# Performance work log

Measured on AMD Instinct MI355X. Metric: run time of the kernel, lower is better.

Reference implementation:

```python
import jax, jax.numpy as jnp
import numpy as np

MAX_DIS = 15
PCD_RANGE = np.array([0.0, 0.0, 0.0, 30.0, 30.0, 14.0])
VOXEL = np.array([2.0, 2.0, 2.0])


def _make_locs():
    low, high = PCD_RANGE[:3], PCD_RANGE[3:]
    grid = ((high - low) // VOXEL + 1).astype(int)  # [16,16,8]
    axes = [low[i] + np.arange(grid[i]) * VOXEL[i] for i in range(3)]
    locs = np.stack(np.meshgrid(*axes, indexing='ij'), axis=-1).reshape(-1, 3)
    return jnp.asarray(locs, jnp.float32)  # [L=2048, 3]


def setup_inputs() -> dict:
    key = jax.random.key(0)
    low, high = PCD_RANGE[:3], PCD_RANGE[3:]
    pcd = jax.random.uniform(key, (4, 8192, 3), dtype=jnp.float32)
    pcd = pcd * jnp.asarray(high - low, jnp.float32) + jnp.asarray(low, jnp.float32)
    return {"pcd": pcd, "locs": _make_locs()}


def reference(pcd, locs):
    # pcd: [B, N, 3]; locs: [L, 3]
    # dis[l, b, n] = ceil(||pcd[b,n] - locs[l]||)
    diff = pcd[None, :, :, :] - locs[:, None, None, :]      # [L, B, N, 3]
    dis = jnp.ceil(jnp.sqrt(jnp.sum(diff * diff, axis=-1)))  # [L, B, N]
    # cumulative distance-threshold counts: feature[t] = #{n : dis <= t+1}
    feats = [jnp.where(dis <= jnp.float32(t + 1), 1.0, 0.0).sum(axis=-1)
             for t in range(MAX_DIS)]                        # each [L, B]
    feature = jnp.stack(feats, axis=0)                       # [MAX_DIS, L, B]
    return feature.transpose(2, 1, 0)                        # [B, L, MAX_DIS]
```

## Files before the change

### kernel.cpp

```cpp
#include <hip/hip_runtime.h>


#define BATCH 4
#define NPTS 8192
#define NLOC 2048
#define NT 15

#if __has_builtin(__builtin_amdgcn_sqrtf)
#define FAST_SQRT(x) __builtin_amdgcn_sqrtf(x)
#else
#define FAST_SQRT(x) sqrtf(x)
#endif

struct f3 { float x, y, z; };

__global__ __launch_bounds__(256, 8) void manual_feature_kernel(
    const float* __restrict__ pcd, const float* __restrict__ locs,
    float* __restrict__ out)
{
    const int tid  = threadIdx.x;
    const int b    = blockIdx.x >> 9;
    const int lt   = blockIdx.x & 511;
    const int loc0 = lt * 4;

    const float lx  = locs[loc0 * 3 + 0];
    const float ly  = locs[loc0 * 3 + 1];
    const float lz0 = locs[loc0 * 3 + 2];
    const float lz1 = locs[loc0 * 3 + 5];
    const float lz2 = locs[loc0 * 3 + 8];
    const float lz3 = locs[loc0 * 3 + 11];

    uint h2[4][4];
#pragma unroll
    for (int j = 0; j < 4; ++j)
#pragma unroll
        for (int w = 0; w < 4; ++w) h2[j][w] = 0u;

    const f3* P = reinterpret_cast<const f3*>(pcd + (size_t)b * NPTS * 3);

    unsigned long long acc0 = 0ull, acc1 = 0ull, acc2 = 0ull, acc3 = 0ull;

#define FOLD()                                                       \
    {                                                                \
        unsigned long long* ap[4] = {&acc0, &acc1, &acc2, &acc3};    \
        _Pragma("unroll")                                            \
        for (int j = 0; j < 4; ++j) {                                \
            const uint lo = (uint)(*ap[j]);                          \
            const uint hi = (uint)(*ap[j] >> 32);                    \
            h2[j][0] += lo & 0x0F0F0F0Fu;                            \
            h2[j][1] += (lo >> 4) & 0x0F0F0F0Fu;                     \
            h2[j][2] += hi & 0x0F0F0F0Fu;                            \
            h2[j][3] += (hi >> 4) & 0x000F0F0Fu; \
            *ap[j] = 0ull;                                           \
        }                                                            \
    }

#pragma unroll
    for (int burst = 0; burst < 8; ++burst) {
        f3 pt[4];
#pragma unroll
        for (int i = 0; i < 4; ++i)
            pt[i] = P[(burst * 4 + i) * 256 + tid];

#pragma unroll
        for (int i = 0; i < 4; ++i) {
            const float dx = pt[i].x - lx;
            const float dy = pt[i].y - ly;
            const float dxy2 = dx * dx + dy * dy;

#define DO_LOC(A, LZ)                                                \
            {                                                        \
                const float dz = pt[i].z - (LZ);                     \
                const float d2 = dz * dz + dxy2;                     \
                const float d  = FAST_SQRT(d2);                      \
                uint f = (uint)d;                                    \
                f = f < 15u ? f : 15u;                               \
                A = (1ull << (f << 2)) + A;      \
            }
            DO_LOC(acc0, lz0)
            DO_LOC(acc1, lz1)
            DO_LOC(acc2, lz2)
            DO_LOC(acc3, lz3)
#undef DO_LOC
        }
        if (burst == 2 || burst == 5 || burst == 7) FOLD()
    }
#undef FOLD

    __shared__ uint smem1[256][17];
#pragma unroll
    for (int j = 0; j < 4; ++j)
#pragma unroll
        for (int w = 0; w < 4; ++w) smem1[tid][j * 4 + w] = h2[j][w];
    __syncthreads();

    __shared__ uint s2lo[4][4][16];
    __shared__ uint s2hi[4][4][16];
    {
        const int loc = tid >> 6, w = (tid >> 4) & 3, ch = tid & 15;
        uint alo = 0u, ahi = 0u;
#pragma unroll
        for (int it = 0; it < 16; ++it) {
            const uint v = smem1[ch * 16 + it][loc * 4 + w];
            alo += v & 0x00FF00FFu;
            ahi += (v >> 8) & 0x00FF00FFu;
        }
        s2lo[loc][w][ch] = alo;
        s2hi[loc][w][ch] = ahi;
    }
    __syncthreads();

    __shared__ uint hfull[4][16];
    if (tid < 64) {
        const int loc = tid >> 4, bkt = tid & 15;
        const int w  = (bkt & 1) + ((bkt >> 3) << 1);
        const int by = (bkt >> 1) & 3;
        const uint* src = (by & 1) ? &s2hi[loc][w][0] : &s2lo[loc][w][0];
        const int sh = (by >> 1) * 16;
        uint s = 0u;
#pragma unroll
        for (int ch = 0; ch < 16; ++ch) s += (src[ch] >> sh) & 0xFFFFu;
        hfull[loc][bkt] = s;
    }
    __syncthreads();

    if (tid < 60) {
        const int loc = tid / 15, t = tid - loc * 15;
        uint s = 0u;
#pragma unroll
        for (int bkt = 0; bkt < NT; ++bkt) s += (bkt <= t) ? hfull[loc][bkt] : 0u;
        out[((size_t)b * NLOC + (size_t)(loc0 + loc)) * NT + t] = (float)s;
    }
}

extern "C" void kernel_launch(void* const* d_in, const int* in_sizes, int n_in,
                              void* d_out, int out_size, void* d_ws, size_t ws_size,
                              hipStream_t stream) {
    const float* pcd  = (const float*)d_in[0];
    const float* locs = (const float*)d_in[1];
    float* out = (float*)d_out;
    manual_feature_kernel<<<dim3(BATCH * (NLOC / 4)), dim3(256), 0, stream>>>(
        pcd, locs, out);
}
```

Measured before the change: 26.81 us.

## Stage point chunks through LDS as SoA and use packed float2 math

Points are now loaded with coalesced float4 reads into LDS, transposed into separate X/Y/Z arrays in chunks of 1024, then read back as float2 pairs so the distance math can use packed 2-wide float ops. The LDS staging buffers share space with the epilogue reduction buffers through a union, and the occupancy hint in launch bounds is dropped. The aim is to remove the strided 12-byte AoS loads and halve the FMA instruction count. In exchange it adds two block barriers per chunk and LDS traffic, and may change occupancy.

```diff
diff --git a/kernel.cpp b/kernel.cpp
--- a/kernel.cpp
+++ b/kernel.cpp
@@ -5,6 +5,10 @@
 #define NPTS 8192
 #define NLOC 2048
 #define NT 15
+#define CH 1024
+#define NCHUNK (NPTS / CH)
+
+typedef float v2f __attribute__((ext_vector_type(2)));
 
 #if __has_builtin(__builtin_amdgcn_sqrtf)
 #define FAST_SQRT(x) __builtin_amdgcn_sqrtf(x)
@@ -12,12 +16,21 @@
 #define FAST_SQRT(x) sqrtf(x)
 #endif
 
-struct f3 { float x, y, z; };
+struct StageBufs { float Xs[CH]; float Ys[CH]; float Zs[CH]; };
+struct EpiBufs {
+    uint smem1[256][17];
+    uint s2lo[4][4][16];
+    uint s2hi[4][4][16];
+    uint hfull[4][16];
+};
+union LdsU { StageBufs s; EpiBufs e; };
 
-__global__ __launch_bounds__(256, 8) void manual_feature_kernel(
+__global__ __launch_bounds__(256) void manual_feature_kernel(
     const float* __restrict__ pcd, const float* __restrict__ locs,
     float* __restrict__ out)
 {
+    __shared__ LdsU L;
+
     const int tid  = threadIdx.x;
     const int b    = blockIdx.x >> 9;
     const int lt   = blockIdx.x & 511;
@@ -25,18 +38,20 @@
 
     const float lx  = locs[loc0 * 3 + 0];
     const float ly  = locs[loc0 * 3 + 1];
-    const float lz0 = locs[loc0 * 3 + 2];
-    const float lz1 = locs[loc0 * 3 + 5];
-    const float lz2 = locs[loc0 * 3 + 8];
-    const float lz3 = locs[loc0 * 3 + 11];
+    const v2f nlx = {-lx, -lx};
+    const v2f nly = {-ly, -ly};
+    v2f nlz[4];
+#pragma unroll
+    for (int j = 0; j < 4; ++j) {
+        const float z = locs[(loc0 + j) * 3 + 2];
+        nlz[j] = (v2f){-z, -z};
+    }
 
     uint h2[4][4];
 #pragma unroll
     for (int j = 0; j < 4; ++j)
 #pragma unroll
         for (int w = 0; w < 4; ++w) h2[j][w] = 0u;
-
-    const f3* P = reinterpret_cast<const f3*>(pcd + (size_t)b * NPTS * 3);
 
     unsigned long long acc0 = 0ull, acc1 = 0ull, acc2 = 0ull, acc3 = 0ull;
 
@@ -55,72 +70,87 @@
         }                                                            \
     }
 
-#pragma unroll
-    for (int burst = 0; burst < 8; ++burst) {
-        f3 pt[4];
-#pragma unroll
-        for (int i = 0; i < 4; ++i)
-            pt[i] = P[(burst * 4 + i) * 256 + tid];
+    const float4* P4 = reinterpret_cast<const float4*>(pcd) + (size_t)b * 6144;
+
+    for (int c = 0; c < NCHUNK; ++c) {
+        {
+            const float4 f0 = P4[c * 768 + 3 * tid + 0];
+            const float4 f1 = P4[c * 768 + 3 * tid + 1];
+            const float4 f2 = P4[c * 768 + 3 * tid + 2];
+            const int p = 4 * tid;
+            L.s.Xs[p + 0] = f0.x; L.s.Xs[p + 1] = f0.w;
+            L.s.Xs[p + 2] = f1.z; L.s.Xs[p + 3] = f2.y;
+            L.s.Ys[p + 0] = f0.y; L.s.Ys[p + 1] = f1.x;
+            L.s.Ys[p + 2] = f1.w; L.s.Ys[p + 3] = f2.z;
+            L.s.Zs[p + 0] = f0.z; L.s.Zs[p + 1] = f1.y;
+            L.s.Zs[p + 2] = f2.x; L.s.Zs[p + 3] = f2.w;
+        }
+        __syncthreads();
 
 #pragma unroll
-        for (int i = 0; i < 4; ++i) {
-            const float dx = pt[i].x - lx;
-            const float dy = pt[i].y - ly;
-            const float dxy2 = dx * dx + dy * dy;
+        for (int it = 0; it < 2; ++it) {
+            const int pi = it * 256 + tid;
+            const v2f x01 = *reinterpret_cast<const v2f*>(&L.s.Xs[2 * pi]);
+            const v2f y01 = *reinterpret_cast<const v2f*>(&L.s.Ys[2 * pi]);
+            const v2f z01 = *reinterpret_cast<const v2f*>(&L.s.Zs[2 * pi]);
 
-#define DO_LOC(A, LZ)                                                \
+            const v2f dx = x01 + nlx;
+            const v2f dy = y01 + nly;
+            v2f dxy = dx * dx;
+            dxy = dy * dy + dxy;
+
+#define DO_LOC(A, J)                                                 \
             {                                                        \
-                const float dz = pt[i].z - (LZ);                     \
-                const float d2 = dz * dz + dxy2;                     \
-                const float d  = FAST_SQRT(d2);                      \
-                uint f = (uint)d;                                    \
-                f = f < 15u ? f : 15u;                               \
-                A = (1ull << (f << 2)) + A;      \
+                const v2f dz = z01 + nlz[J];                         \
+                const v2f d2 = dz * dz + dxy;            \
+                uint fa = (uint)FAST_SQRT(d2.x);                     \
+                uint fb = (uint)FAST_SQRT(d2.y);                     \
+                fa = fa < 15u ? fa : 15u;                            \
+                fb = fb < 15u ? fb : 15u;                            \
+                A = (1ull << (fa << 2)) + A;                         \
+                A = (1ull << (fb << 2)) + A;                         \
             }
-            DO_LOC(acc0, lz0)
-            DO_LOC(acc1, lz1)
-            DO_LOC(acc2, lz2)
-            DO_LOC(acc3, lz3)
+            DO_LOC(acc0, 0)
+            DO_LOC(acc1, 1)
+            DO_LOC(acc2, 2)
+            DO_LOC(acc3, 3)
 #undef DO_LOC
         }
-        if (burst == 2 || burst == 5 || burst == 7) FOLD()
+        if (c == 2 || c == 5 || c == 7) FOLD()
+        __syncthreads();
     }
 #undef FOLD
 
-    __shared__ uint smem1[256][17];
 #pragma unroll
     for (int j = 0; j < 4; ++j)
 #pragma unroll
-        for (int w = 0; w < 4; ++w) smem1[tid][j * 4 + w] = h2[j][w];
+        for (int w = 0; w < 4; ++w) L.e.smem1[tid][j * 4 + w] = h2[j][w];
     __syncthreads();
 
-    __shared__ uint s2lo[4][4][16];
-    __shared__ uint s2hi[4][4][16];
     {
         const int loc = tid >> 6, w = (tid >> 4) & 3, ch = tid & 15;
         uint alo = 0u, ahi = 0u;
 #pragma unroll
         for (int it = 0; it < 16; ++it) {
-            const uint v = smem1[ch * 16 + it][loc * 4 + w];
+            const uint v = L.e.smem1[ch * 16 + it][loc * 4 + w];
             alo += v & 0x00FF00FFu;
             ahi += (v >> 8) & 0x00FF00FFu;
         }
-        s2lo[loc][w][ch] = alo;
-        s2hi[loc][w][ch] = ahi;
+        L.e.s2lo[loc][w][ch] = alo;
+        L.e.s2hi[loc][w][ch] = ahi;
     }
     __syncthreads();
 
-    __shared__ uint hfull[4][16];
     if (tid < 64) {
         const int loc = tid >> 4, bkt = tid & 15;
         const int w  = (bkt & 1) + ((bkt >> 3) << 1);
         const int by = (bkt >> 1) & 3;
-        const uint* src = (by & 1) ? &s2hi[loc][w][0] : &s2lo[loc][w][0];
+        const uint* src = (by & 1) ? &L.e.s2hi[loc][w][0] : &L.e.s2lo[loc][w][0];
         const int sh = (by >> 1) * 16;
         uint s = 0u;
 #pragma unroll
         for (int ch = 0; ch < 16; ++ch) s += (src[ch] >> sh) & 0xFFFFu;
-        hfull[loc][bkt] = s;
+        L.e.hfull[loc][bkt] = s;
     }
     __syncthreads();
 
@@ -128,7 +158,7 @@
         const int loc = tid / 15, t = tid - loc * 15;
         uint s = 0u;
 #pragma unroll
-        for (int bkt = 0; bkt < NT; ++bkt) s += (bkt <= t) ? hfull[loc][bkt] : 0u;
+        for (int bkt = 0; bkt < NT; ++bkt) s += (bkt <= t) ? L.e.hfull[loc][bkt] : 0u;
         out[((size_t)b * NLOC + (size_t)(loc0 + loc)) * NT + t] = (float)s;
     }
 }
```

Result: slower. 33.97 us (+26.7%).
